# Performance work log

Measured on AMD Instinct MI355X. Metric: run time of the kernel, lower is better.

## Reference

```python
import jax, jax.numpy as jnp
import numpy as np

B, T, D, H, HD = 2, 2048, 1024, 16, 64


def setup_inputs() -> dict:
    key = jax.random.key(0)
    kx, kq, kk, kv, ko = jax.random.split(key, 5)
    s = 1.0 / np.sqrt(D)
    return {
        "x": jax.random.normal(kx, (B, T, D), dtype=jnp.float32),
        "Wq": jax.random.normal(kq, (H, D, HD), dtype=jnp.float32) * s,
        "Wk": jax.random.normal(kk, (H, D, HD), dtype=jnp.float32) * s,
        "Wv": jax.random.normal(kv, (H, D, HD), dtype=jnp.float32) * s,
        "Wo": jax.random.normal(ko, (D, D), dtype=jnp.float32) * s,
        "bo": jnp.zeros((D,), dtype=jnp.float32),
    }


def reference(x, Wq, Wk, Wv, Wo, bo):
    # Batched equivalent of the per-head loop: q/k/v for all heads at once.
    q = jnp.einsum("btd,hdk->bhtk", x, Wq)  # [B,H,T,HD]
    k = jnp.einsum("btd,hdk->bhtk", x, Wk)
    v = jnp.einsum("btd,hdk->bhtk", x, Wv)
    scale = 1.0 / jnp.sqrt(jnp.asarray(HD, dtype=x.dtype))
    scores = jnp.einsum("bhqk,bhsk->bhqs", q, k) * scale  # [B,H,T,T]
    causal = jnp.tril(jnp.ones((T, T), dtype=bool))
    scores = jnp.where(causal, scores, jnp.asarray(-1e9, dtype=scores.dtype))
    attn = jax.nn.softmax(scores, axis=-1)
    out = jnp.einsum("bhqs,bhsk->bhqk", attn, v)  # [B,H,T,HD]
    out = out.transpose(0, 2, 1, 3).reshape(B, T, H * HD)  # concat heads
    return out @ Wo + bo  # dropout is identity in eval (p used at train only)
```

## Files before the change

### kernel.cpp

```cpp
#include <hip/hip_runtime.h>
#include <hip/hip_bf16.h>
#include <stdint.h>
#include <stddef.h>

typedef __bf16 bf16_t;
typedef __attribute__((ext_vector_type(4))) __bf16 bf16x4;
typedef __attribute__((ext_vector_type(8))) __bf16 bf16x8;
typedef __attribute__((ext_vector_type(4))) float floatx4;

#define GLD16(gp, lp) __builtin_amdgcn_global_load_lds(                      \
    (__attribute__((address_space(1))) void*)(gp),                           \
    (__attribute__((address_space(3))) void*)(lp), 16, 0, 0)

__global__ __launch_bounds__(256) void prep(
    const float* __restrict__ x, const float* __restrict__ Wq,
    const float* __restrict__ Wk, const float* __restrict__ Wv,
    const float* __restrict__ Wo, bf16_t* __restrict__ XB,
    bf16_t* __restrict__ WT, bf16_t* __restrict__ WoT) {
  __shared__ bf16_t t[64][65];
  int bx = blockIdx.x;
  const int tid = threadIdx.x;
  if (bx < 2048) {
    const int i = (bx * 256 + tid) * 8;
    const float4 v0 = *(const float4*)(x + i);
    const float4 v1 = *(const float4*)(x + i + 4);
    bf16x8 o = {(bf16_t)v0.x, (bf16_t)v0.y, (bf16_t)v0.z, (bf16_t)v0.w,
                (bf16_t)v1.x, (bf16_t)v1.y, (bf16_t)v1.z, (bf16_t)v1.w};
    *(bf16x8*)(XB + i) = o;
    return;
  }
  bx -= 2048;
  const int g = tid >> 6, l = tid & 63;
  if (bx < 768) {
    const int d0 = (bx & 15) * 64, h = (bx >> 4) & 15, z = bx >> 8;
    const float* W = (z == 0) ? Wq : (z == 1) ? Wk : Wv;
    const float* src = W + (size_t)h * 65536 + (size_t)d0 * 64;
    #pragma unroll
    for (int i = 0; i < 16; ++i) { int r = g * 16 + i; t[r][l] = (bf16_t)src[(size_t)r * 64 + l]; }
    __syncthreads();
    bf16_t* dst = WT + ((size_t)z * 1024 + h * 64) * 1024 + d0;
    #pragma unroll
    for (int i = 0; i < 16; ++i) { int c = g * 16 + i; dst[(size_t)c * 1024 + l] = t[l][c]; }
  } else {
    bx -= 768;
    const int r0 = (bx & 15) * 64, c0 = (bx >> 4) * 64;
    #pragma unroll
    for (int i = 0; i < 16; ++i) { int r = g * 16 + i; t[r][l] = (bf16_t)Wo[(size_t)(r0 + r) * 1024 + c0 + l]; }
    __syncthreads();
    #pragma unroll
    for (int i = 0; i < 16; ++i) { int c = g * 16 + i; WoT[(size_t)(c0 + c) * 1024 + r0 + l] = t[l][c]; }
  }
}

template <bool BIAS, typename OutT>
__device__ __forceinline__ void gemm_body(
    const bf16_t* __restrict__ A, const bf16_t* __restrict__ Bt,
    OutT* __restrict__ C, const float* __restrict__ bias,
    int K, int lda, int ldb, int ldc, int m0, int n0,
    bf16_t* As, bf16_t* Bs) {
  const int tid = threadIdx.x;
  const int lane = tid & 63, w = tid >> 6;
  const int qd = lane >> 4, ln = lane & 15;
  const int wm = (w & 1) * 64, wn = (w >> 1) * 64;

  const floatx4 z4 = {0.f, 0.f, 0.f, 0.f};
  floatx4 acc[4][4];
  #pragma unroll
  for (int i = 0; i < 4; ++i)
    #pragma unroll
    for (int j = 0; j < 4; ++j) acc[i][j] = z4;

  for (int k0 = 0; k0 < K; k0 += 32) {
    #pragma unroll
    for (int i = 0; i < 2; ++i) {
      const int c = tid + i * 256;
      const int row = c >> 2, slot = c & 3;
      GLD16(A + (size_t)(m0 + row) * lda + k0 + slot * 8, As + (size_t)(w * 64 + i * 256) * 8);
      GLD16(Bt + (size_t)(n0 + row) * ldb + k0 + slot * 8, Bs + (size_t)(w * 64 + i * 256) * 8);
    }
    __syncthreads();
    bf16x8 af[4], bfr[4];
    #pragma unroll
    for (int t = 0; t < 4; ++t) {
      af[t]  = *(const bf16x8*)(As + (wm + t * 16 + ln) * 32 + qd * 8);
      bfr[t] = *(const bf16x8*)(Bs + (wn + t * 16 + ln) * 32 + qd * 8);
    }
    #pragma unroll
    for (int mt = 0; mt < 4; ++mt)
      #pragma unroll
      for (int nt = 0; nt < 4; ++nt)
        acc[mt][nt] = __builtin_amdgcn_mfma_f32_16x16x32_bf16(af[mt], bfr[nt], acc[mt][nt], 0, 0, 0);
    __syncthreads();
  }

  #pragma unroll
  for (int nt = 0; nt < 4; ++nt) {
    const int col = n0 + wn + nt * 16 + ln;
    const float bv = BIAS ? bias[col] : 0.f;
    #pragma unroll
    for (int mt = 0; mt < 4; ++mt) {
      const int row = m0 + wm + mt * 16 + qd * 4;
      #pragma unroll
      for (int r = 0; r < 4; ++r)
        C[(size_t)(row + r) * ldc + col] = (OutT)(acc[mt][nt][r] + bv);
    }
  }
}

__global__ __launch_bounds__(256) void proj_gemm(
    const bf16_t* __restrict__ XB, const bf16_t* __restrict__ WT,
    bf16_t* __restrict__ C1, bf16_t* __restrict__ VT) {
  __shared__ __align__(16) bf16_t As[128 * 32];
  __shared__ __align__(16) bf16_t Bs[128 * 32];
  int bx = blockIdx.x;
  if (bx < 512) {
    gemm_body<false, bf16_t>(XB, WT, C1, nullptr, 1024, 1024, 1024, 2048,
                             (bx & 31) * 128, (bx >> 5) * 128, As, Bs);
  } else {
    bx -= 512;
    gemm_body<false, bf16_t>(WT + (size_t)2048 * 1024, XB, VT, nullptr,
                             1024, 1024, 1024, 4096,
                             (bx & 7) * 128, (bx >> 3) * 128, As, Bs);
  }
}

__global__ __launch_bounds__(256) void out_gemm(
    const bf16_t* __restrict__ AO, const bf16_t* __restrict__ WoT,
    float* __restrict__ C, const float* __restrict__ bias) {
  __shared__ __align__(16) bf16_t As[128 * 32];
  __shared__ __align__(16) bf16_t Bs[128 * 32];
  gemm_body<true, float>(AO, WoT, C, bias, 1024, 1024, 1024, 1024,
                         blockIdx.x * 128, blockIdx.y * 128, As, Bs);
}

__global__ __launch_bounds__(256) void flash_attn(
    const bf16_t* __restrict__ C1, const bf16_t* __restrict__ VT,
    bf16_t* __restrict__ AO) {
  constexpr int LDK = 72;
  __shared__ __align__(16) bf16_t Ks[2][64 * LDK];
  __shared__ __align__(16) bf16_t Vs[2][64 * LDK];
  __shared__ __align__(16) bf16_t Psa[4][16 * LDK];
  __shared__ __align__(16) bf16_t Psb[4][16 * LDK];
  const int qta = blockIdx.x, qtb = 31 - (int)blockIdx.x;
  const int h = blockIdx.y, b = blockIdx.z;
  const int tid = threadIdx.x, lane = tid & 63, w = tid >> 6;
  const int qd = lane >> 4, ln = lane & 15;
  const bf16_t* Qb = C1 + (size_t)b * 2048 * 2048;

  bf16x8 qa0, qa1, qb0, qb1;
  {
    const bf16_t* qp = Qb + (size_t)(qta * 64 + w * 16 + ln) * 2048 + h * 64 + qd * 8;
    qa0 = *(const bf16x8*)qp;
    qa1 = *(const bf16x8*)(qp + 32);
    qp = Qb + (size_t)(qtb * 64 + w * 16 + ln) * 2048 + h * 64 + qd * 8;
    qb0 = *(const bf16x8*)qp;
    qb1 = *(const bf16x8*)(qp + 32);
  }
  float lsum_a = 0.f, lsum_b = 0.f;
  const floatx4 z4 = {0.f, 0.f, 0.f, 0.f};
  floatx4 oacc_a[4], oacc_b[4];
  #pragma unroll
  for (int t = 0; t < 4; ++t) { oacc_a[t] = z4; oacc_b[t] = z4; }

  const bf16_t* Kg = Qb + 1024 + h * 64;
  const bf16_t* Vg = VT + (size_t)(h * 64) * 4096 + b * 2048;
  const float SCL = 0.18033688011112042f;

  const int c0 = tid, c1 = tid + 256;
  const int r0s = c0 >> 3, s0s = (c0 & 7) * 8;
  const int r1s = c1 >> 3, s1s = (c1 & 7) * 8;

  bf16x8 kr0, kr1, vr0, vr1;
  {
    kr0 = *(const bf16x8*)(Kg + (size_t)r0s * 2048 + s0s);
    kr1 = *(const bf16x8*)(Kg + (size_t)r1s * 2048 + s1s);
    vr0 = *(const bf16x8*)(Vg + (size_t)r0s * 4096 + s0s);
    vr1 = *(const bf16x8*)(Vg + (size_t)r1s * 4096 + s1s);
    *(bf16x8*)(&Ks[0][r0s * LDK + s0s]) = kr0;
    *(bf16x8*)(&Ks[0][r1s * LDK + s1s]) = kr1;
    *(bf16x8*)(&Vs[0][r0s * LDK + s0s]) = vr0;
    *(bf16x8*)(&Vs[0][r1s * LDK + s1s]) = vr1;
  }
  __syncthreads();

  for (int st = 0; st <= qtb; ++st) {
    const int bi = st & 1;
    const bool doA = (st <= qta);
    if (st < qtb) {
      const int s0 = (st + 1) * 64;
      kr0 = *(const bf16x8*)(Kg + (size_t)(s0 + r0s) * 2048 + s0s);
      kr1 = *(const bf16x8*)(Kg + (size_t)(s0 + r1s) * 2048 + s1s);
      vr0 = *(const bf16x8*)(Vg + (size_t)r0s * 4096 + s0 + s0s);
      vr1 = *(const bf16x8*)(Vg + (size_t)r1s * 4096 + s0 + s1s);
    }

    floatx4 sa[4], sb[4];
    #pragma unroll
    for (int nt = 0; nt < 4; ++nt) {
      const bf16_t* kp = &Ks[bi][(nt * 16 + ln) * LDK + qd * 8];
      bf16x8 kf0 = *(const bf16x8*)kp;
      bf16x8 kf1 = *(const bf16x8*)(kp + 32);
      floatx4 t0 = z4;
      t0 = __builtin_amdgcn_mfma_f32_16x16x32_bf16(kf0, qb0, t0, 0, 0, 0);
      t0 = __builtin_amdgcn_mfma_f32_16x16x32_bf16(kf1, qb1, t0, 0, 0, 0);
      sb[nt] = t0;
      if (doA) {
        floatx4 t1 = z4;
        t1 = __builtin_amdgcn_mfma_f32_16x16x32_bf16(kf0, qa0, t1, 0, 0, 0);
        t1 = __builtin_amdgcn_mfma_f32_16x16x32_bf16(kf1, qa1, t1, 0, 0, 0);
        sa[nt] = t1;
      }
    }

    {
      float rs = 0.f;
      #pragma unroll
      for (int nt = 0; nt < 4; ++nt) {
        float p[4];
        #pragma unroll
        for (int r = 0; r < 4; ++r) {
          float v = sb[nt][r] * SCL;
          if (st == qtb && (nt * 16 + qd * 4 + r) > (w * 16 + ln)) v = -1e30f;
          p[r] = __builtin_amdgcn_exp2f(v);
          rs += p[r];
        }
        bf16x4 pk = {(bf16_t)p[0], (bf16_t)p[1], (bf16_t)p[2], (bf16_t)p[3]};
        *(bf16x4*)(&Psb[w][ln * LDK + nt * 16 + qd * 4]) = pk;
      }
      rs += __shfl_xor(rs, 16);
      rs += __shfl_xor(rs, 32);
      lsum_b += rs;
    }
    if (doA) {
      float rs = 0.f;
      #pragma unroll
      for (int nt = 0; nt < 4; ++nt) {
        float p[4];
        #pragma unroll
        for (int r = 0; r < 4; ++r) {
          float v = sa[nt][r] * SCL;
          if (st == qta && (nt * 16 + qd * 4 + r) > (w * 16 + ln)) v = -1e30f;
          p[r] = __builtin_amdgcn_exp2f(v);
          rs += p[r];
        }
        bf16x4 pk = {(bf16_t)p[0], (bf16_t)p[1], (bf16_t)p[2], (bf16_t)p[3]};
        *(bf16x4*)(&Psa[w][ln * LDK + nt * 16 + qd * 4]) = pk;
      }
      rs += __shfl_xor(rs, 16);
      rs += __shfl_xor(rs, 32);
      lsum_a += rs;
    }

    bf16x8 pb0 = *(const bf16x8*)(&Psb[w][ln * LDK + qd * 8]);
    bf16x8 pb1 = *(const bf16x8*)(&Psb[w][ln * LDK + 32 + qd * 8]);
    bf16x8 pa0, pa1;
    if (doA) {
      pa0 = *(const bf16x8*)(&Psa[w][ln * LDK + qd * 8]);
      pa1 = *(const bf16x8*)(&Psa[w][ln * LDK + 32 + qd * 8]);
    }
    #pragma unroll
    for (int t = 0; t < 4; ++t) {
      const bf16_t* vp = &Vs[bi][(t * 16 + ln) * LDK + qd * 8];
      bf16x8 vf0 = *(const bf16x8*)vp;
      bf16x8 vf1 = *(const bf16x8*)(vp + 32);
      oacc_b[t] = __builtin_amdgcn_mfma_f32_16x16x32_bf16(pb0, vf0, oacc_b[t], 0, 0, 0);
      oacc_b[t] = __builtin_amdgcn_mfma_f32_16x16x32_bf16(pb1, vf1, oacc_b[t], 0, 0, 0);
      if (doA) {
        oacc_a[t] = __builtin_amdgcn_mfma_f32_16x16x32_bf16(pa0, vf0, oacc_a[t], 0, 0, 0);
        oacc_a[t] = __builtin_amdgcn_mfma_f32_16x16x32_bf16(pa1, vf1, oacc_a[t], 0, 0, 0);
      }
    }

    if (st < qtb) {
      const int ni = (st + 1) & 1;
      *(bf16x8*)(&Ks[ni][r0s * LDK + s0s]) = kr0;
      *(bf16x8*)(&Ks[ni][r1s * LDK + s1s]) = kr1;
      *(bf16x8*)(&Vs[ni][r0s * LDK + s0s]) = vr0;
      *(bf16x8*)(&Vs[ni][r1s * LDK + s1s]) = vr1;
    }
    __syncthreads();
  }

  const float rla = 1.0f / lsum_a, rlb = 1.0f / lsum_b;
  #pragma unroll
  for (int r = 0; r < 4; ++r) {
    const float la = __shfl(rla, qd * 4 + r);
    const float lb = __shfl(rlb, qd * 4 + r);
    #pragma unroll
    for (int t = 0; t < 4; ++t) {
      const int col = h * 64 + t * 16 + ln;
      const int rowa = b * 2048 + qta * 64 + w * 16 + qd * 4 + r;
      const int rowb = b * 2048 + qtb * 64 + w * 16 + qd * 4 + r;
      AO[(size_t)rowa * 1024 + col] = (bf16_t)(oacc_a[t][r] * la);
      AO[(size_t)rowb * 1024 + col] = (bf16_t)(oacc_b[t][r] * lb);
    }
  }
}

extern "C" void kernel_launch(void* const* d_in, const int* in_sizes, int n_in,
                              void* d_out, int out_size, void* d_ws, size_t ws_size,
                              hipStream_t stream) {
  const float* x  = (const float*)d_in[0];
  const float* Wq = (const float*)d_in[1];
  const float* Wk = (const float*)d_in[2];
  const float* Wv = (const float*)d_in[3];
  const float* Wo = (const float*)d_in[4];
  const float* bo = (const float*)d_in[5];
  float* out = (float*)d_out;

  bf16_t* WT  = (bf16_t*)d_ws;
  bf16_t* WoT = WT + (size_t)3072 * 1024;
  bf16_t* C1  = WoT + (size_t)1024 * 1024;
  bf16_t* AO  = C1 + (size_t)4096 * 2048;
  bf16_t* XB  = (bf16_t*)d_out;
  bf16_t* VT  = XB + (size_t)4096 * 1024;

  prep<<<dim3(3072), 256, 0, stream>>>(x, Wq, Wk, Wv, Wo, XB, WT, WoT);
  proj_gemm<<<dim3(768), 256, 0, stream>>>(XB, WT, C1, VT);
  flash_attn<<<dim3(16, 16, 2), 256, 0, stream>>>(C1, VT, AO);
  out_gemm<<<dim3(32, 8), 256, 0, stream>>>(AO, WoT, out, bo);
}
```

Before: 205.0 us.

## Double GEMM K-tile to 64 with XOR-swizzled LDS and share P buffer

The GEMM main loop now stages 64-wide K slices per iteration instead of 32. This halves the number of barrier pairs and loads, and the LDS layout uses an XOR swizzle on 16-byte segments to avoid bank conflicts on fragment reads. In the attention kernel the two P staging buffers are merged into one, with the B tile's fragments read back before the A tile overwrites the buffer, to cut LDS footprint. The trade-off is doubled GEMM shared memory per block and a serialised read-before-overwrite dependency on the shared P buffer.

Result: faster. 190.9 us (-6.9%).

```diff
diff --git a/kernel.cpp b/kernel.cpp
--- a/kernel.cpp
+++ b/kernel.cpp
@@ -70,26 +70,32 @@
     #pragma unroll
     for (int j = 0; j < 4; ++j) acc[i][j] = z4;
 
-  for (int k0 = 0; k0 < K; k0 += 32) {
-    #pragma unroll
-    for (int i = 0; i < 2; ++i) {
+  for (int k0 = 0; k0 < K; k0 += 64) {
+    #pragma unroll
+    for (int i = 0; i < 4; ++i) {
       const int c = tid + i * 256;
-      const int row = c >> 2, slot = c & 3;
-      GLD16(A + (size_t)(m0 + row) * lda + k0 + slot * 8, As + (size_t)(w * 64 + i * 256) * 8);
-      GLD16(Bt + (size_t)(n0 + row) * ldb + k0 + slot * 8, Bs + (size_t)(w * 64 + i * 256) * 8);
-    }
-    __syncthreads();
-    bf16x8 af[4], bfr[4];
-    #pragma unroll
-    for (int t = 0; t < 4; ++t) {
-      af[t]  = *(const bf16x8*)(As + (wm + t * 16 + ln) * 32 + qd * 8);
-      bfr[t] = *(const bf16x8*)(Bs + (wn + t * 16 + ln) * 32 + qd * 8);
-    }
-    #pragma unroll
-    for (int mt = 0; mt < 4; ++mt)
-      #pragma unroll
-      for (int nt = 0; nt < 4; ++nt)
-        acc[mt][nt] = __builtin_amdgcn_mfma_f32_16x16x32_bf16(af[mt], bfr[nt], acc[mt][nt], 0, 0, 0);
+      const int row = c >> 3;
+      const int sg = (c & 7) ^ (row & 7);
+      GLD16(A + (size_t)(m0 + row) * lda + k0 + sg * 8, As + (size_t)(w * 64 + i * 256) * 8);
+      GLD16(Bt + (size_t)(n0 + row) * ldb + k0 + sg * 8, Bs + (size_t)(w * 64 + i * 256) * 8);
+    }
+    __syncthreads();
+    #pragma unroll
+    for (int h = 0; h < 2; ++h) {
+      bf16x8 af[4], bfr[4];
+      #pragma unroll
+      for (int t = 0; t < 4; ++t) {
+        const int ra = wm + t * 16 + ln;
+        const int rb = wn + t * 16 + ln;
+        af[t]  = *(const bf16x8*)(As + (size_t)ra * 64 + (((h * 4 + qd) ^ (ra & 7)) * 8));
+        bfr[t] = *(const bf16x8*)(Bs + (size_t)rb * 64 + (((h * 4 + qd) ^ (rb & 7)) * 8));
+      }
+      #pragma unroll
+      for (int mt = 0; mt < 4; ++mt)
+        #pragma unroll
+        for (int nt = 0; nt < 4; ++nt)
+          acc[mt][nt] = __builtin_amdgcn_mfma_f32_16x16x32_bf16(af[mt], bfr[nt], acc[mt][nt], 0, 0, 0);
+    }
     __syncthreads();
   }
 
@@ -110,8 +116,8 @@
 __global__ __launch_bounds__(256) void proj_gemm(
     const bf16_t* __restrict__ XB, const bf16_t* __restrict__ WT,
     bf16_t* __restrict__ C1, bf16_t* __restrict__ VT) {
-  __shared__ __align__(16) bf16_t As[128 * 32];
-  __shared__ __align__(16) bf16_t Bs[128 * 32];
+  __shared__ __align__(16) bf16_t As[128 * 64];
+  __shared__ __align__(16) bf16_t Bs[128 * 64];
   int bx = blockIdx.x;
   if (bx < 512) {
     gemm_body<false, bf16_t>(XB, WT, C1, nullptr, 1024, 1024, 1024, 2048,
@@ -127,8 +133,8 @@
 __global__ __launch_bounds__(256) void out_gemm(
     const bf16_t* __restrict__ AO, const bf16_t* __restrict__ WoT,
     float* __restrict__ C, const float* __restrict__ bias) {
-  __shared__ __align__(16) bf16_t As[128 * 32];
-  __shared__ __align__(16) bf16_t Bs[128 * 32];
+  __shared__ __align__(16) bf16_t As[128 * 64];
+  __shared__ __align__(16) bf16_t Bs[128 * 64];
   gemm_body<true, float>(AO, WoT, C, bias, 1024, 1024, 1024, 1024,
                          blockIdx.x * 128, blockIdx.y * 128, As, Bs);
 }
@@ -139,8 +145,7 @@
   constexpr int LDK = 72;
   __shared__ __align__(16) bf16_t Ks[2][64 * LDK];
   __shared__ __align__(16) bf16_t Vs[2][64 * LDK];
-  __shared__ __align__(16) bf16_t Psa[4][16 * LDK];
-  __shared__ __align__(16) bf16_t Psb[4][16 * LDK];
+  __shared__ __align__(16) bf16_t Ps[4][16 * LDK];
   const int qta = blockIdx.x, qtb = 31 - (int)blockIdx.x;
   const int h = blockIdx.y, b = blockIdx.z;
   const int tid = threadIdx.x, lane = tid & 63, w = tid >> 6;
@@ -225,12 +230,16 @@
           rs += p[r];
         }
         bf16x4 pk = {(bf16_t)p[0], (bf16_t)p[1], (bf16_t)p[2], (bf16_t)p[3]};
-        *(bf16x4*)(&Psb[w][ln * LDK + nt * 16 + qd * 4]) = pk;
+        *(bf16x4*)(&Ps[w][ln * LDK + nt * 16 + qd * 4]) = pk;
       }
       rs += __shfl_xor(rs, 16);
       rs += __shfl_xor(rs, 32);
       lsum_b += rs;
     }
+    bf16x8 pb0 = *(const bf16x8*)(&Ps[w][ln * LDK + qd * 8]);
+    bf16x8 pb1 = *(const bf16x8*)(&Ps[w][ln * LDK + 32 + qd * 8]);
+
+    bf16x8 pa0, pa1;
     if (doA) {
       float rs = 0.f;
       #pragma unroll
@@ -244,20 +253,15 @@
           rs += p[r];
         }
         bf16x4 pk = {(bf16_t)p[0], (bf16_t)p[1], (bf16_t)p[2], (bf16_t)p[3]};
-        *(bf16x4*)(&Psa[w][ln * LDK + nt * 16 + qd * 4]) = pk;
+        *(bf16x4*)(&Ps[w][ln * LDK + nt * 16 + qd * 4]) = pk;
       }
       rs += __shfl_xor(rs, 16);
       rs += __shfl_xor(rs, 32);
       lsum_a += rs;
-    }
-
-    bf16x8 pb0 = *(const bf16x8*)(&Psb[w][ln * LDK + qd * 8]);
-    bf16x8 pb1 = *(const bf16x8*)(&Psb[w][ln * LDK + 32 + qd * 8]);
-    bf16x8 pa0, pa1;
-    if (doA) {
-      pa0 = *(const bf16x8*)(&Psa[w][ln * LDK + qd * 8]);
-      pa1 = *(const bf16x8*)(&Psa[w][ln * LDK + 32 + qd * 8]);
-    }
+      pa0 = *(const bf16x8*)(&Ps[w][ln * LDK + qd * 8]);
+      pa1 = *(const bf16x8*)(&Ps[w][ln * LDK + 32 + qd * 8]);
+    }
+
     #pragma unroll
     for (int t = 0; t < 4; ++t) {
       const bf16_t* vp = &Vs[bi][(t * 16 + ln) * LDK + qd * 8];
```
